# Optimization experiments

Hardware: AMD Instinct MI355X
Metric: run time of the kernel (lower is better)

Reference implementation:

```python
import jax, jax.numpy as jnp
import numpy as np

B, L, D = 8, 2048, 256
NEG = 10000.0


def setup_inputs() -> dict:
    key = jax.random.key(0)
    kq, kk, kv, km = jax.random.split(key, 4)
    return {
        "query": jax.random.normal(kq, (B, L, D), dtype=jnp.float32),
        "key": jax.random.normal(kk, (B, L, D), dtype=jnp.float32),
        "value": jax.random.normal(kv, (B, L, D), dtype=jnp.float32),
        "mask": jax.random.randint(km, (B, L), 0, 2).astype(bool),
    }


def reference(query, key, value, mask):
    d = query.shape[-1]
    # scores: [B, Lq, Lk]
    e = jnp.einsum("bqd,bkd->bqk", query, key) / jnp.sqrt(jnp.asarray(d, query.dtype))
    # history_only (causal) mask: subtract 10000 where key index > query index
    q_len, k_len = query.shape[1], key.shape[1]
    causal = (jnp.arange(k_len)[None, :] > jnp.arange(q_len)[:, None]).astype(query.dtype)
    e = e - NEG * causal[None, :, :]
    # key padding mask: [B, 1, Lk]
    e = e - NEG * (1.0 - mask.astype(query.dtype))[:, None, :]
    attn = jax.nn.softmax(e, axis=-1)
    return jnp.einsum("bqk,bkd->bqd", attn, value)
```

## Files before the change

### kernel.cpp

```cpp
#include <hip/hip_runtime.h>
#include <stdint.h>

#define NL 2048
#define ND 256
#define KVB 32
#define QB 64
#define NQT 32
#define NT_ALL (NL / KVB)
#define CHUNK 10
#define NCHUNKS_B 125
#define TILE_BYTES (KVB * ND * 2)
#define IMG (8 * NT_ALL * TILE_BYTES)
#define WS_MB 256
#define WS_K (WS_MB + 2048)
#define WS_V (WS_K + IMG)
#define WS_P (WS_V + IMG)
#define PART_BYTES (QB * ND * 2 + QB * 8)

typedef __attribute__((ext_vector_type(8))) short short8;
typedef __attribute__((ext_vector_type(4))) short short4v;
typedef __attribute__((ext_vector_type(4))) float f32x4;
typedef __attribute__((ext_vector_type(4))) unsigned int u32x4;
typedef __attribute__((ext_vector_type(8))) unsigned short ushort8;

__device__ __forceinline__ unsigned short bf16rne(float x) {
  unsigned u = __builtin_bit_cast(unsigned, x);
  u += 0x7FFFu + ((u >> 16) & 1u);
  return (unsigned short)(u >> 16);
}

__device__ __forceinline__ short8 cvt8(float4 a, float4 b, float scale) {
  short8 v;
  v[0] = (short)bf16rne(a.x * scale);
  v[1] = (short)bf16rne(a.y * scale);
  v[2] = (short)bf16rne(a.z * scale);
  v[3] = (short)bf16rne(a.w * scale);
  v[4] = (short)bf16rne(b.x * scale);
  v[5] = (short)bf16rne(b.y * scale);
  v[6] = (short)bf16rne(b.z * scale);
  v[7] = (short)bf16rne(b.w * scale);
  return v;
}

__global__ __launch_bounds__(128)
void convert_kv(const float* __restrict__ K, const float* __restrict__ V,
                const unsigned* __restrict__ M, unsigned char* __restrict__ ws) {
  if (blockIdx.x == 512) {
    __shared__ int badS;
    if (threadIdx.x == 0) badS = 0;
    __syncthreads();
    bool bad = false;
    for (int i = threadIdx.x; i < 4096; i += 128)
      if (M[i] > 1u) bad = true;
    if (__any(bad) && (threadIdx.x & 63) == 0) badS = 1;
    __syncthreads();
    const int byteMode = badS;
    unsigned* MB = (unsigned*)(ws + WS_MB);
    for (int t = threadIdx.x; t < 512; t += 128) {
      unsigned m = 0;
      for (int j = 0; j < 32; ++j) {
        int mv = byteMode ? (int)((const unsigned char*)M)[t * 32 + j]
                          : (int)M[t * 32 + j];
        m |= (mv ? 1u : 0u) << j;
      }
      MB[t] = m;
    }
    return;
  }
  const int t = blockIdx.x;
  const int b = t >> 6, tix = t & 63;
  const float* kt = K + ((size_t)b * NL + tix * KVB) * ND;
  const float* vt = V + ((size_t)b * NL + tix * KVB) * ND;
  unsigned char* kd = ws + WS_K + (size_t)t * TILE_BYTES;
  unsigned char* vd = ws + WS_V + (size_t)t * TILE_BYTES;
#pragma unroll
  for (int it = 0; it < 8; ++it) {
    int idx = it * 128 + threadIdx.x;
    int row = idx >> 5, u = idx & 31, f = u * 8;
    const float4* kp = (const float4*)(kt + (size_t)row * ND + f);
    int kb = (row * 512 + f * 2) ^ ((row & 7) << 4);
    *(short8*)(kd + kb) = cvt8(kp[0], kp[1], 1.0f);
    const float4* vp = (const float4*)(vt + (size_t)row * ND + f);
    int vb = (row >> 2) * 2048 + (u >> 1) * 128 + (row & 3) * 32 + (u & 1) * 16;
    *(short8*)(vd + vb) = cvt8(vp[0], vp[1], 1.0f);
  }
}

__global__ __launch_bounds__(256, 2)
void attn_fwd(const float* __restrict__ Qg, const unsigned* __restrict__ MBg,
              unsigned char* ws) {
  __shared__ unsigned short Ks[3][KVB * ND];
  __shared__ unsigned short Vs[2][KVB * ND];

  const int tid = threadIdx.x;
  const int wv = tid >> 6;
  const int lane = tid & 63;
  const int g = lane >> 4;
  const int cc = lane & 15;

  const int fid = blockIdx.x;
  const int b = fid / NCHUNKS_B;
  int rem = fid - b * NCHUNKS_B;
  int qt = 0, c = 0, pbase = 0;
  if (rem < 7) {
    qt = 0; c = rem; pbase = 0;
  } else {
    rem -= 7; pbase = 7;
    for (qt = 1; qt < NQT; ++qt) {
      int ncq = (2 * qt + 2 + CHUNK - 1) / CHUNK;
      if (rem < ncq) { c = rem; break; }
      rem -= ncq; pbase += ncq;
    }
  }
  const int qb = qt * QB;
  const int nt_s = (qt == 0) ? NT_ALL : (2 * qt + 2);
  const int t0 = c * CHUNK;
  const int t1 = min(nt_s, t0 + CHUNK);
  unsigned char* pp = ws + WS_P + (size_t)(b * NCHUNKS_B + pbase + c) * PART_BYTES;
  unsigned short* ppA = (unsigned short*)pp;
  float* ppM = (float*)(pp + QB * ND * 2);
  float* ppL = ppM + QB;

  auto stage_K = [&](int tix, int bi) {
    const unsigned char* kg = ws + WS_K + ((size_t)(b * NT_ALL + tix)) * TILE_BYTES;
#pragma unroll
    for (int s = 0; s < 4; ++s) {
      const int seg = wv * 4 + s;
      __builtin_amdgcn_global_load_lds(
          (const __attribute__((address_space(1))) unsigned int*)(kg + seg * 1024 + lane * 16),
          (__attribute__((address_space(3))) unsigned int*)((unsigned char*)&Ks[bi][0] + seg * 1024),
          16, 0, 0);
    }
  };
  auto stage_V = [&](int tix, int bi) {
    const unsigned char* vg = ws + WS_V + ((size_t)(b * NT_ALL + tix)) * TILE_BYTES;
#pragma unroll
    for (int s = 0; s < 4; ++s) {
      const int seg = wv * 4 + s;
      __builtin_amdgcn_global_load_lds(
          (const __attribute__((address_space(1))) unsigned int*)(vg + seg * 1024 + lane * 16),
          (__attribute__((address_space(3))) unsigned int*)((unsigned char*)&Vs[bi][0] + seg * 1024),
          16, 0, 0);
    }
  };

  const float* qp = Qg + ((size_t)b * NL + (qb + 16 * wv + cc)) * ND;
  short8 qf[8];
#pragma unroll
  for (int ch = 0; ch < 8; ++ch) {
    int f = ch * 32 + g * 8;
    float4 a0 = *reinterpret_cast<const float4*>(qp + f);
    float4 a1 = *reinterpret_cast<const float4*>(qp + f + 4);
    qf[ch] = cvt8(a0, a1, 0.0625f);
  }
  const int qg = qb + 16 * wv + cc;

  f32x4 acc[16];
#pragma unroll
  for (int i = 0; i < 16; ++i) acc[i] = (f32x4){0.f, 0.f, 0.f, 0.f};
  float m_run = -3.0e38f, l_run = 0.f;

  asm volatile("s_waitcnt vmcnt(0)" ::: "memory");
  __builtin_amdgcn_sched_barrier(0);
  stage_K(t0, t0 % 3);
  stage_V(t0, t0 & 1);
  if (t0 + 1 < t1) stage_K(t0 + 1, (t0 + 1) % 3);

  for (int tix = t0; tix < t1; ++tix) {
    if (tix + 1 < t1) {
      asm volatile("s_waitcnt vmcnt(4)" ::: "memory");
    } else {
      asm volatile("s_waitcnt vmcnt(0)" ::: "memory");
    }
    __builtin_amdgcn_sched_barrier(0);
    __builtin_amdgcn_s_barrier();
    __builtin_amdgcn_sched_barrier(0);
    if (tix + 1 < t1) stage_V(tix + 1, (tix + 1) & 1);
    if (tix + 2 < t1) stage_K(tix + 2, (tix + 2) % 3);

    const int kv0 = tix * KVB;
    const unsigned mb = MBg[b * NT_ALL + tix];

    const char* ksB = (const char*)&Ks[tix % 3][0];
    f32x4 s0 = {0.f, 0.f, 0.f, 0.f}, s1 = {0.f, 0.f, 0.f, 0.f};
    __builtin_amdgcn_s_setprio(1);
#pragma unroll
    for (int ch = 0; ch < 8; ++ch) {
      int cbase = ch * 64 + g * 16;
      int b0 = (cc * 512 + cbase) ^ ((cc & 7) << 4);
      int b1 = ((cc + 16) * 512 + cbase) ^ ((cc & 7) << 4);
      short8 k0 = *reinterpret_cast<const short8*>(ksB + b0);
      short8 k1 = *reinterpret_cast<const short8*>(ksB + b1);
      s0 = __builtin_amdgcn_mfma_f32_16x16x32_bf16(k0, qf[ch], s0, 0, 0, 0);
      s1 = __builtin_amdgcn_mfma_f32_16x16x32_bf16(k1, qf[ch], s1, 0, 0, 0);
    }
    __builtin_amdgcn_s_setprio(0);

#pragma unroll
    for (int r = 0; r < 4; ++r) {
      int k0i = 4 * g + r, k1i = 16 + 4 * g + r;
      if (!((mb >> k0i) & 1u)) s0[r] -= 10000.f;
      if (!((mb >> k1i) & 1u)) s1[r] -= 10000.f;
      if (kv0 + k0i > qg) s0[r] -= 10000.f;
      if (kv0 + k1i > qg) s1[r] -= 10000.f;
    }

    float rmax = fmaxf(fmaxf(fmaxf(s0[0], s0[1]), fmaxf(s0[2], s0[3])),
                       fmaxf(fmaxf(s1[0], s1[1]), fmaxf(s1[2], s1[3])));
    rmax = fmaxf(rmax, __shfl_xor(rmax, 16));
    rmax = fmaxf(rmax, __shfl_xor(rmax, 32));
    bool grow = (rmax > m_run + 8.f);
    if (__any(grow)) {
      float mn = fmaxf(m_run, rmax);
      float alpha = __expf(m_run - mn);
      m_run = mn;
      l_run *= alpha;
      f32x4 av;
#pragma unroll
      for (int r = 0; r < 4; ++r) av[r] = __shfl(alpha, 20 * g + r);
#pragma unroll
      for (int i = 0; i < 16; ++i) acc[i] *= av;
    }
    float p0[4], p1[4];
#pragma unroll
    for (int r = 0; r < 4; ++r) {
      p0[r] = __expf(s0[r] - m_run);
      p1[r] = __expf(s1[r] - m_run);
    }
    l_run += (p0[0] + p0[1]) + (p0[2] + p0[3]) +
             (p1[0] + p1[1]) + (p1[2] + p1[3]);

    unsigned a0, a1, b0w, b1w;
    asm("v_cvt_pk_bf16_f32 %0, %1, %2" : "=v"(a0) : "v"(p0[0]), "v"(p0[1]));
    asm("v_cvt_pk_bf16_f32 %0, %1, %2" : "=v"(a1) : "v"(p0[2]), "v"(p0[3]));
    asm("v_cvt_pk_bf16_f32 %0, %1, %2" : "=v"(b0w) : "v"(p1[0]), "v"(p1[1]));
    asm("v_cvt_pk_bf16_f32 %0, %1, %2" : "=v"(b1w) : "v"(p1[2]), "v"(p1[3]));
    const int srcLo = cc + ((g & 1) << 5);
    const int srcHi = srcLo + 16;
    unsigned wa0 = (unsigned)__shfl((int)a0, srcLo);
    unsigned wa1 = (unsigned)__shfl((int)a1, srcLo);
    unsigned wa2 = (unsigned)__shfl((int)a0, srcHi);
    unsigned wa3 = (unsigned)__shfl((int)a1, srcHi);
    unsigned wb0 = (unsigned)__shfl((int)b0w, srcLo);
    unsigned wb1 = (unsigned)__shfl((int)b1w, srcLo);
    unsigned wb2 = (unsigned)__shfl((int)b0w, srcHi);
    unsigned wb3 = (unsigned)__shfl((int)b1w, srcHi);
    const bool hiHalf = (g >= 2);
    u32x4 paw = {hiHalf ? wb0 : wa0, hiHalf ? wb1 : wa1,
                 hiHalf ? wb2 : wa2, hiHalf ? wb3 : wa3};
    short8 pa = __builtin_bit_cast(short8, paw);

    const unsigned va = (unsigned)(uintptr_t)&Vs[tix & 1][0] + g * 4096 + cc * 8;
    short4v lo[16], hi[16];
#pragma unroll
    for (int ft = 0; ft < 16; ++ft) {
      asm volatile("ds_read_b64_tr_b16 %0, %1 offset:%2"
                   : "=&v"(lo[ft]) : "v"(va), "i"(ft * 128) : "memory");
      asm volatile("ds_read_b64_tr_b16 %0, %1 offset:%2"
                   : "=&v"(hi[ft]) : "v"(va), "i"(ft * 128 + 2048) : "memory");
    }
    asm volatile("s_waitcnt lgkmcnt(15)" ::: "memory");
    __builtin_amdgcn_sched_barrier(0);
    __builtin_amdgcn_s_setprio(1);
#pragma unroll
    for (int ft = 0; ft < 8; ++ft) {
      short8 vb = __builtin_shufflevector(lo[ft], hi[ft], 0, 1, 2, 3, 4, 5, 6, 7);
      acc[ft] = __builtin_amdgcn_mfma_f32_16x16x32_bf16(pa, vb, acc[ft], 0, 0, 0);
    }
    __builtin_amdgcn_s_setprio(0);
    asm volatile("s_waitcnt lgkmcnt(0)" ::: "memory");
    __builtin_amdgcn_sched_barrier(0);
    __builtin_amdgcn_s_setprio(1);
#pragma unroll
    for (int ft = 8; ft < 16; ++ft) {
      short8 vb = __builtin_shufflevector(lo[ft], hi[ft], 0, 1, 2, 3, 4, 5, 6, 7);
      acc[ft] = __builtin_amdgcn_mfma_f32_16x16x32_bf16(pa, vb, acc[ft], 0, 0, 0);
    }
    __builtin_amdgcn_s_setprio(0);
  }

  l_run += __shfl_xor(l_run, 16);
  l_run += __shfl_xor(l_run, 32);

  __syncthreads();
  unsigned short* sc = &Ks[0][0];
#pragma unroll
  for (int ft = 0; ft < 16; ++ft) {
#pragma unroll
    for (int r = 0; r < 4; ++r) {
      sc[(16 * wv + 4 * g + r) * 256 + ft * 16 + cc] = bf16rne(acc[ft][r]);
    }
  }
  if (g == 0) {
    ppM[16 * wv + cc] = m_run;
    ppL[16 * wv + cc] = l_run;
  }
  __syncthreads();
  {
    const int row = tid >> 2, q4 = tid & 3;
    const unsigned short* srow = sc + row * 256 + q4 * 64;
#pragma unroll
    for (int kk = 0; kk < 8; ++kk) {
      *(ushort8*)(ppA + (size_t)row * ND + q4 * 64 + kk * 8) =
          *(const ushort8*)(srow + kk * 8);
    }
  }
}

__global__ __launch_bounds__(256)
void attn_combine(const unsigned char* __restrict__ ws, float* __restrict__ Og) {
  const int bid = blockIdx.x;
  const int b = bid >> 7;
  const int qt = (bid >> 2) & 31;
  const int qu = bid & 3;
  const int tid = threadIdx.x;
  const int row = qu * 16 + (tid >> 4);
  const int colb = (tid & 15) * 16;

  int pbase = 0, nc = 7;
  if (qt > 0) {
    pbase = 7;
    for (int j = 1; j < qt; ++j) pbase += (2 * j + 2 + CHUNK - 1) / CHUNK;
    nc = (2 * qt + 2 + CHUNK - 1) / CHUNK;
  }
  const unsigned char* p0 = ws + WS_P + (size_t)(b * NCHUNKS_B + pbase) * PART_BYTES;

  float M = -3.0e38f;
  for (int c = 0; c < nc; ++c) {
    M = fmaxf(M, *(const float*)(p0 + (size_t)c * PART_BYTES + QB * ND * 2 + row * 4));
  }
  float L = 0.f;
  float o[16];
#pragma unroll
  for (int j = 0; j < 16; ++j) o[j] = 0.f;
  for (int c = 0; c < nc; ++c) {
    const unsigned char* pc = p0 + (size_t)c * PART_BYTES;
    float mm = *(const float*)(pc + QB * ND * 2 + row * 4);
    float ll = *(const float*)(pc + QB * ND * 2 + QB * 4 + row * 4);
    float s = __expf(mm - M);
    L += ll * s;
    const unsigned short* pa =
        (const unsigned short*)pc + (size_t)row * ND + colb;
#pragma unroll
    for (int kk = 0; kk < 2; ++kk) {
      ushort8 a = *(const ushort8*)(pa + kk * 8);
#pragma unroll
      for (int j = 0; j < 8; ++j) {
        unsigned u = ((unsigned)a[j]) << 16;
        o[kk * 8 + j] += __builtin_bit_cast(float, u) * s;
      }
    }
  }
  const float invL = 1.0f / L;
  float* op = Og + ((size_t)b * NL + qt * QB + row) * ND + colb;
#pragma unroll
  for (int kk = 0; kk < 4; ++kk) {
    float4 v = {o[kk * 4] * invL, o[kk * 4 + 1] * invL, o[kk * 4 + 2] * invL,
                o[kk * 4 + 3] * invL};
    *(float4*)(op + kk * 4) = v;
  }
}

extern "C" void kernel_launch(void* const* d_in, const int* in_sizes, int n_in,
                              void* d_out, int out_size, void* d_ws, size_t ws_size,
                              hipStream_t stream) {
  (void)in_sizes; (void)n_in; (void)out_size; (void)ws_size;
  const float* Q = (const float*)d_in[0];
  const float* K = (const float*)d_in[1];
  const float* V = (const float*)d_in[2];
  const int* M = (const int*)d_in[3];
  unsigned char* ws = (unsigned char*)d_ws;

  convert_kv<<<dim3(513), dim3(128), 0, stream>>>(K, V, (const unsigned*)M, ws);
  attn_fwd<<<dim3(8 * NCHUNKS_B), dim3(256), 0, stream>>>(
      Q, (const unsigned*)(ws + WS_MB), ws);
  attn_combine<<<dim3(1024), dim3(256), 0, stream>>>(ws, (float*)d_out);
}
```

Baseline: 95.58 us.

## Switch attention to 32x32x16 MFMA with 128-row query tiles

Doubles the query tile per block to 128 rows, with 32 rows per wave, and replaces the 16x16x32 bf16 MFMAs with 32x32x16 MFMAs for both QK^T and PV. This halves K/V LDS traffic per query row and removes the cross-lane shuffles that built the P operand. V transpose reads are now double-buffered, interleaved with the MFMAs. Chunking and the combine kernel are re-derived for the new tile size. In exchange, fewer blocks are launched and each thread carries more accumulator registers, which risks lower occupancy and worse load balance.

```diff
diff --git a/kernel.cpp b/kernel.cpp
--- a/kernel.cpp
+++ b/kernel.cpp
@@ -4,11 +4,11 @@
 #define NL 2048
 #define ND 256
 #define KVB 32
-#define QB 64
-#define NQT 32
+#define QB 128
+#define NPAIR 16
 #define NT_ALL (NL / KVB)
-#define CHUNK 10
-#define NCHUNKS_B 125
+#define CHUNK 11
+#define NCHUNKS_B 62
 #define TILE_BYTES (KVB * ND * 2)
 #define IMG (8 * NT_ALL * TILE_BYTES)
 #define WS_MB 256
@@ -19,7 +19,7 @@
 
 typedef __attribute__((ext_vector_type(8))) short short8;
 typedef __attribute__((ext_vector_type(4))) short short4v;
-typedef __attribute__((ext_vector_type(4))) float f32x4;
+typedef __attribute__((ext_vector_type(16))) float f32x16;
 typedef __attribute__((ext_vector_type(4))) unsigned int u32x4;
 typedef __attribute__((ext_vector_type(8))) unsigned short ushort8;
 
@@ -95,25 +95,27 @@
   const int tid = threadIdx.x;
   const int wv = tid >> 6;
   const int lane = tid & 63;
-  const int g = lane >> 4;
-  const int cc = lane & 15;
+  const int l31 = lane & 31;
+  const int h = lane >> 5;
+  const int g16 = (lane >> 4) & 1;
+  const int c16 = lane & 15;
 
   const int fid = blockIdx.x;
   const int b = fid / NCHUNKS_B;
   int rem = fid - b * NCHUNKS_B;
-  int qt = 0, c = 0, pbase = 0;
-  if (rem < 7) {
-    qt = 0; c = rem; pbase = 0;
+  int j = 0, c = 0, pbase = 0;
+  if (rem < 6) {
+    j = 0; c = rem; pbase = 0;
   } else {
-    rem -= 7; pbase = 7;
-    for (qt = 1; qt < NQT; ++qt) {
-      int ncq = (2 * qt + 2 + CHUNK - 1) / CHUNK;
+    rem -= 6; pbase = 6;
+    for (j = 1; j < NPAIR; ++j) {
+      int ncq = (4 * j + 4 + CHUNK - 1) / CHUNK;
       if (rem < ncq) { c = rem; break; }
       rem -= ncq; pbase += ncq;
     }
   }
-  const int qb = qt * QB;
-  const int nt_s = (qt == 0) ? NT_ALL : (2 * qt + 2);
+  const int qb = j * QB;
+  const int nt_s = (j == 0) ? NT_ALL : (4 * j + 4);
   const int t0 = c * CHUNK;
   const int t1 = min(nt_s, t0 + CHUNK);
   unsigned char* pp = ws + WS_P + (size_t)(b * NCHUNKS_B + pbase + c) * PART_BYTES;
@@ -144,20 +146,20 @@
     }
   };
 
-  const float* qp = Qg + ((size_t)b * NL + (qb + 16 * wv + cc)) * ND;
-  short8 qf[8];
-#pragma unroll
-  for (int ch = 0; ch < 8; ++ch) {
-    int f = ch * 32 + g * 8;
+  const float* qp = Qg + ((size_t)b * NL + (qb + 32 * wv + l31)) * ND;
+  short8 qf[16];
+#pragma unroll
+  for (int ch = 0; ch < 16; ++ch) {
+    int f = ch * 16 + h * 8;
     float4 a0 = *reinterpret_cast<const float4*>(qp + f);
     float4 a1 = *reinterpret_cast<const float4*>(qp + f + 4);
     qf[ch] = cvt8(a0, a1, 0.0625f);
   }
-  const int qg = qb + 16 * wv + cc;
-
-  f32x4 acc[16];
-#pragma unroll
-  for (int i = 0; i < 16; ++i) acc[i] = (f32x4){0.f, 0.f, 0.f, 0.f};
+  const int qg = qb + 32 * wv + l31;
+
+  f32x16 acc[8];
+#pragma unroll
+  for (int i = 0; i < 8; ++i) acc[i] = (f32x16)(0.f);
   float m_run = -3.0e38f, l_run = 0.f;
 
   asm volatile("s_waitcnt vmcnt(0)" ::: "memory");
@@ -166,6 +168,8 @@
   stage_V(t0, t0 & 1);
   if (t0 + 1 < t1) stage_K(t0 + 1, (t0 + 1) % 3);
 
+  const int swzK = (l31 & 7) << 4;
+
   for (int tix = t0; tix < t1; ++tix) {
     if (tix + 1 < t1) {
       asm volatile("s_waitcnt vmcnt(4)" ::: "memory");
@@ -182,32 +186,26 @@
     const unsigned mb = MBg[b * NT_ALL + tix];
 
     const char* ksB = (const char*)&Ks[tix % 3][0];
-    f32x4 s0 = {0.f, 0.f, 0.f, 0.f}, s1 = {0.f, 0.f, 0.f, 0.f};
+    f32x16 s = (f32x16)(0.f);
     __builtin_amdgcn_s_setprio(1);
 #pragma unroll
-    for (int ch = 0; ch < 8; ++ch) {
-      int cbase = ch * 64 + g * 16;
-      int b0 = (cc * 512 + cbase) ^ ((cc & 7) << 4);
-      int b1 = ((cc + 16) * 512 + cbase) ^ ((cc & 7) << 4);
-      short8 k0 = *reinterpret_cast<const short8*>(ksB + b0);
-      short8 k1 = *reinterpret_cast<const short8*>(ksB + b1);
-      s0 = __builtin_amdgcn_mfma_f32_16x16x32_bf16(k0, qf[ch], s0, 0, 0, 0);
-      s1 = __builtin_amdgcn_mfma_f32_16x16x32_bf16(k1, qf[ch], s1, 0, 0, 0);
+    for (int ch = 0; ch < 16; ++ch) {
+      int kb = (l31 * 512 + ch * 32 + h * 16) ^ swzK;
+      short8 kf = *reinterpret_cast<const short8*>(ksB + kb);
+      s = __builtin_amdgcn_mfma_f32_32x32x16_bf16(kf, qf[ch], s, 0, 0, 0);
     }
     __builtin_amdgcn_s_setprio(0);
 
 #pragma unroll
-    for (int r = 0; r < 4; ++r) {
-      int k0i = 4 * g + r, k1i = 16 + 4 * g + r;
-      if (!((mb >> k0i) & 1u)) s0[r] -= 10000.f;
-      if (!((mb >> k1i) & 1u)) s1[r] -= 10000.f;
-      if (kv0 + k0i > qg) s0[r] -= 10000.f;
-      if (kv0 + k1i > qg) s1[r] -= 10000.f;
-    }
-
-    float rmax = fmaxf(fmaxf(fmaxf(s0[0], s0[1]), fmaxf(s0[2], s0[3])),
-                       fmaxf(fmaxf(s1[0], s1[1]), fmaxf(s1[2], s1[3])));
-    rmax = fmaxf(rmax, __shfl_xor(rmax, 16));
+    for (int r = 0; r < 16; ++r) {
+      int kvi = (r & 3) + 8 * (r >> 2) + 4 * h;
+      if (!((mb >> kvi) & 1u)) s[r] -= 10000.f;
+      if (kv0 + kvi > qg) s[r] -= 10000.f;
+    }
+
+    float rmax = s[0];
+#pragma unroll
+    for (int r = 1; r < 16; ++r) rmax = fmaxf(rmax, s[r]);
     rmax = fmaxf(rmax, __shfl_xor(rmax, 32));
     bool grow = (rmax > m_run + 8.f);
     if (__any(grow)) {
@@ -215,93 +213,103 @@
       float alpha = __expf(m_run - mn);
       m_run = mn;
       l_run *= alpha;
-      f32x4 av;
-#pragma unroll
-      for (int r = 0; r < 4; ++r) av[r] = __shfl(alpha, 20 * g + r);
-#pragma unroll
-      for (int i = 0; i < 16; ++i) acc[i] *= av;
-    }
-    float p0[4], p1[4];
-#pragma unroll
-    for (int r = 0; r < 4; ++r) {
-      p0[r] = __expf(s0[r] - m_run);
-      p1[r] = __expf(s1[r] - m_run);
-    }
-    l_run += (p0[0] + p0[1]) + (p0[2] + p0[3]) +
-             (p1[0] + p1[1]) + (p1[2] + p1[3]);
-
-    unsigned a0, a1, b0w, b1w;
-    asm("v_cvt_pk_bf16_f32 %0, %1, %2" : "=v"(a0) : "v"(p0[0]), "v"(p0[1]));
-    asm("v_cvt_pk_bf16_f32 %0, %1, %2" : "=v"(a1) : "v"(p0[2]), "v"(p0[3]));
-    asm("v_cvt_pk_bf16_f32 %0, %1, %2" : "=v"(b0w) : "v"(p1[0]), "v"(p1[1]));
-    asm("v_cvt_pk_bf16_f32 %0, %1, %2" : "=v"(b1w) : "v"(p1[2]), "v"(p1[3]));
-    const int srcLo = cc + ((g & 1) << 5);
-    const int srcHi = srcLo + 16;
-    unsigned wa0 = (unsigned)__shfl((int)a0, srcLo);
-    unsigned wa1 = (unsigned)__shfl((int)a1, srcLo);
-    unsigned wa2 = (unsigned)__shfl((int)a0, srcHi);
-    unsigned wa3 = (unsigned)__shfl((int)a1, srcHi);
-    unsigned wb0 = (unsigned)__shfl((int)b0w, srcLo);
-    unsigned wb1 = (unsigned)__shfl((int)b1w, srcLo);
-    unsigned wb2 = (unsigned)__shfl((int)b0w, srcHi);
-    unsigned wb3 = (unsigned)__shfl((int)b1w, srcHi);
-    const bool hiHalf = (g >= 2);
-    u32x4 paw = {hiHalf ? wb0 : wa0, hiHalf ? wb1 : wa1,
-                 hiHalf ? wb2 : wa2, hiHalf ? wb3 : wa3};
-    short8 pa = __builtin_bit_cast(short8, paw);
-
-    const unsigned va = (unsigned)(uintptr_t)&Vs[tix & 1][0] + g * 4096 + cc * 8;
-    short4v lo[16], hi[16];
-#pragma unroll
-    for (int ft = 0; ft < 16; ++ft) {
-      asm volatile("ds_read_b64_tr_b16 %0, %1 offset:%2"
-                   : "=&v"(lo[ft]) : "v"(va), "i"(ft * 128) : "memory");
-      asm volatile("ds_read_b64_tr_b16 %0, %1 offset:%2"
-                   : "=&v"(hi[ft]) : "v"(va), "i"(ft * 128 + 2048) : "memory");
-    }
-    asm volatile("s_waitcnt lgkmcnt(15)" ::: "memory");
-    __builtin_amdgcn_sched_barrier(0);
-    __builtin_amdgcn_s_setprio(1);
-#pragma unroll
-    for (int ft = 0; ft < 8; ++ft) {
-      short8 vb = __builtin_shufflevector(lo[ft], hi[ft], 0, 1, 2, 3, 4, 5, 6, 7);
-      acc[ft] = __builtin_amdgcn_mfma_f32_16x16x32_bf16(pa, vb, acc[ft], 0, 0, 0);
-    }
-    __builtin_amdgcn_s_setprio(0);
-    asm volatile("s_waitcnt lgkmcnt(0)" ::: "memory");
-    __builtin_amdgcn_sched_barrier(0);
-    __builtin_amdgcn_s_setprio(1);
-#pragma unroll
-    for (int ft = 8; ft < 16; ++ft) {
-      short8 vb = __builtin_shufflevector(lo[ft], hi[ft], 0, 1, 2, 3, 4, 5, 6, 7);
-      acc[ft] = __builtin_amdgcn_mfma_f32_16x16x32_bf16(pa, vb, acc[ft], 0, 0, 0);
-    }
-    __builtin_amdgcn_s_setprio(0);
-  }
-
-  l_run += __shfl_xor(l_run, 16);
+      f32x16 av;
+#pragma unroll
+      for (int r = 0; r < 16; ++r)
+        av[r] = __shfl(alpha, (r & 3) + 8 * (r >> 2) + 4 * h);
+#pragma unroll
+      for (int i = 0; i < 8; ++i) acc[i] *= av;
+    }
+    float p[16];
+    float ls = 0.f;
+#pragma unroll
+    for (int r = 0; r < 16; ++r) {
+      p[r] = __expf(s[r] - m_run);
+      ls += p[r];
+    }
+    l_run += ls;
+
+    unsigned w0, w1, w2, w3, w4, w5, w6, w7;
+    asm("v_cvt_pk_bf16_f32 %0, %1, %2" : "=v"(w0) : "v"(p[0]), "v"(p[1]));
+    asm("v_cvt_pk_bf16_f32 %0, %1, %2" : "=v"(w1) : "v"(p[2]), "v"(p[3]));
+    asm("v_cvt_pk_bf16_f32 %0, %1, %2" : "=v"(w2) : "v"(p[4]), "v"(p[5]));
+    asm("v_cvt_pk_bf16_f32 %0, %1, %2" : "=v"(w3) : "v"(p[6]), "v"(p[7]));
+    asm("v_cvt_pk_bf16_f32 %0, %1, %2" : "=v"(w4) : "v"(p[8]), "v"(p[9]));
+    asm("v_cvt_pk_bf16_f32 %0, %1, %2" : "=v"(w5) : "v"(p[10]), "v"(p[11]));
+    asm("v_cvt_pk_bf16_f32 %0, %1, %2" : "=v"(w6) : "v"(p[12]), "v"(p[13]));
+    asm("v_cvt_pk_bf16_f32 %0, %1, %2" : "=v"(w7) : "v"(p[14]), "v"(p[15]));
+    short8 pa0 = __builtin_bit_cast(short8, (u32x4){w0, w1, w2, w3});
+    short8 pa1 = __builtin_bit_cast(short8, (u32x4){w4, w5, w6, w7});
+
+    const unsigned va = (unsigned)(uintptr_t)&Vs[tix & 1][0] +
+                        (unsigned)(c16 * 8 + g16 * 128 + h * 2048);
+    short4v trA[4], trB[4];
+#define TR_ISSUE(buf, DD)                                                      \
+  asm volatile("ds_read_b64_tr_b16 %0, %1 offset:%2"                          \
+               : "=&v"(buf[0]) : "v"(va), "i"((DD)*256) : "memory");           \
+  asm volatile("ds_read_b64_tr_b16 %0, %1 offset:%2"                          \
+               : "=&v"(buf[1]) : "v"(va), "i"((DD)*256 + 4096) : "memory");    \
+  asm volatile("ds_read_b64_tr_b16 %0, %1 offset:%2"                          \
+               : "=&v"(buf[2]) : "v"(va), "i"((DD)*256 + 8192) : "memory");    \
+  asm volatile("ds_read_b64_tr_b16 %0, %1 offset:%2"                          \
+               : "=&v"(buf[3]) : "v"(va), "i"((DD)*256 + 12288) : "memory")
+
+    TR_ISSUE(trA, 0);
+#pragma unroll
+    for (int dd = 0; dd < 8; ++dd) {
+      if (dd & 1) {
+        if (dd < 7) { TR_ISSUE(trA, dd + 1); }
+        if (dd < 7) { asm volatile("s_waitcnt lgkmcnt(4)" ::: "memory"); }
+        else        { asm volatile("s_waitcnt lgkmcnt(0)" ::: "memory"); }
+        __builtin_amdgcn_sched_barrier(0);
+        short8 vb0 = __builtin_shufflevector(trB[0], trB[1], 0, 1, 2, 3, 4, 5, 6, 7);
+        short8 vb1 = __builtin_shufflevector(trB[2], trB[3], 0, 1, 2, 3, 4, 5, 6, 7);
+        __builtin_amdgcn_s_setprio(1);
+        acc[dd] = __builtin_amdgcn_mfma_f32_32x32x16_bf16(pa0, vb0, acc[dd], 0, 0, 0);
+        acc[dd] = __builtin_amdgcn_mfma_f32_32x32x16_bf16(pa1, vb1, acc[dd], 0, 0, 0);
+        __builtin_amdgcn_s_setprio(0);
+      } else {
+        if (dd < 7) { TR_ISSUE(trB, dd + 1); }
+        if (dd < 7) { asm volatile("s_waitcnt lgkmcnt(4)" ::: "memory"); }
+        else        { asm volatile("s_waitcnt lgkmcnt(0)" ::: "memory"); }
+        __builtin_amdgcn_sched_barrier(0);
+        short8 vb0 = __builtin_shufflevector(trA[0], trA[1], 0, 1, 2, 3, 4, 5, 6, 7);
+        short8 vb1 = __builtin_shufflevector(trA[2], trA[3], 0, 1, 2, 3, 4, 5, 6, 7);
+        __builtin_amdgcn_s_setprio(1);
+        acc[dd] = __builtin_amdgcn_mfma_f32_32x32x16_bf16(pa0, vb0, acc[dd], 0, 0, 0);
+        acc[dd] = __builtin_amdgcn_mfma_f32_32x32x16_bf16(pa1, vb1, acc[dd], 0, 0, 0);
+        __builtin_amdgcn_s_setprio(0);
+      }
+    }
+#undef TR_ISSUE
+  }
+
   l_run += __shfl_xor(l_run, 32);
-
-  __syncthreads();
+  if (h == 0) {
+    ppM[wv * 32 + l31] = m_run;
+    ppL[wv * 32 + l31] = l_run;
+  }
+
   unsigned short* sc = &Ks[0][0];
 #pragma unroll
-  for (int ft = 0; ft < 16; ++ft) {
-#pragma unroll
-    for (int r = 0; r < 4; ++r) {
-      sc[(16 * wv + 4 * g + r) * 256 + ft * 16 + cc] = bf16rne(acc[ft][r]);
-    }
-  }
-  if (g == 0) {
-    ppM[16 * wv + cc] = m_run;
-    ppL[16 * wv + cc] = l_run;
-  }
-  __syncthreads();
-  {
+  for (int hh = 0; hh < 2; ++hh) {
+    __syncthreads();
+    if ((wv >> 1) == hh) {
+#pragma unroll
+      for (int dd = 0; dd < 8; ++dd) {
+#pragma unroll
+        for (int r = 0; r < 16; ++r) {
+          int qr = (r & 3) + 8 * (r >> 2) + 4 * h;
+          sc[((wv & 1) * 32 + qr) * 256 + dd * 32 + l31] = bf16rne(acc[dd][r]);
+        }
+      }
+    }
+    __syncthreads();
     const int row = tid >> 2, q4 = tid & 3;
     const unsigned short* srow = sc + row * 256 + q4 * 64;
 #pragma unroll
     for (int kk = 0; kk < 8; ++kk) {
-      *(ushort8*)(ppA + (size_t)row * ND + q4 * 64 + kk * 8) =
+      *(ushort8*)(ppA + (size_t)(hh * 64 + row) * ND + q4 * 64 + kk * 8) =
           *(const ushort8*)(srow + kk * 8);
     }
   }
@@ -311,17 +319,17 @@
 void attn_combine(const unsigned char* __restrict__ ws, float* __restrict__ Og) {
   const int bid = blockIdx.x;
   const int b = bid >> 7;
-  const int qt = (bid >> 2) & 31;
-  const int qu = bid & 3;
+  const int j = (bid >> 3) & 15;
+  const int qu = bid & 7;
   const int tid = threadIdx.x;
   const int row = qu * 16 + (tid >> 4);
   const int colb = (tid & 15) * 16;
 
-  int pbase = 0, nc = 7;
-  if (qt > 0) {
-    pbase = 7;
-    for (int j = 1; j < qt; ++j) pbase += (2 * j + 2 + CHUNK - 1) / CHUNK;
-    nc = (2 * qt + 2 + CHUNK - 1) / CHUNK;
+  int pbase = 0, nc = 6;
+  if (j > 0) {
+    pbase = 6;
+    for (int jj = 1; jj < j; ++jj) pbase += (4 * jj + 4 + CHUNK - 1) / CHUNK;
+    nc = (4 * j + 4 + CHUNK - 1) / CHUNK;
   }
   const unsigned char* p0 = ws + WS_P + (size_t)(b * NCHUNKS_B + pbase) * PART_BYTES;
 
@@ -332,27 +340,26 @@
   float L = 0.f;
   float o[16];
 #pragma unroll
-  for (int j = 0; j < 16; ++j) o[j] = 0.f;
+  for (int q = 0; q < 16; ++q) o[q] = 0.f;
   for (int c = 0; c < nc; ++c) {
     const unsigned char* pc = p0 + (size_t)c * PART_BYTES;
     float mm = *(const float*)(pc + QB * ND * 2 + row * 4);
     float ll = *(const float*)(pc + QB * ND * 2 + QB * 4 + row * 4);
-    float s = __expf(mm - M);
-    L += ll * s;
-    const unsigned short* pa =
-        (const unsigned short*)pc + (size_t)row * ND + colb;
+    float sc = __expf(mm - M);
+    L += ll * sc;
+    const unsigned short* pa = (const unsigned short*)pc + (size_t)row * ND + colb;
 #pragma unroll
     for (int kk = 0; kk < 2; ++kk) {
       ushort8 a = *(const ushort8*)(pa + kk * 8);
 #pragma unroll
-      for (int j = 0; j < 8; ++j) {
-        unsigned u = ((unsigned)a[j]) << 16;
-        o[kk * 8 + j] += __builtin_bit_cast(float, u) * s;
+      for (int q = 0; q < 8; ++q) {
+        unsigned u = ((unsigned)a[q]) << 16;
+        o[kk * 8 + q] += __builtin_bit_cast(float, u) * sc;
       }
     }
   }
   const float invL = 1.0f / L;
-  float* op = Og + ((size_t)b * NL + qt * QB + row) * ND + colb;
+  float* op = Og + ((size_t)b * NL + j * QB + row) * ND + colb;
 #pragma unroll
   for (int kk = 0; kk < 4; ++kk) {
     float4 v = {o[kk * 4] * invL, o[kk * 4 + 1] * invL, o[kk * 4 + 2] * invL,
```

New measurement: 99.26 us. 1.04x slower.
